# Kernel tuning notes

Measured on AMD Instinct MI355X. Metric: run time of the kernel, lower is better.

## Reference

```python
import jax, jax.numpy as jnp
import numpy as np

NEG_INF = jnp.float32(-jnp.inf)


def setup_inputs() -> dict:
    key = jax.random.key(0)
    k1, k2, k3, k4 = jax.random.split(key, 4)
    B, QL, H = 16, 32, 128          # batch, query tokens, embed dim
    N_DOCS, DL = 20000, 64          # documents, doc tokens per doc
    N_CAND = 1024                   # candidate embeddings per query
    N_EMB = N_DOCS * DL
    return {
        "q_vectors": jax.random.normal(k1, (B, QL, H), dtype=jnp.float32),
        "topk_indices": jax.random.randint(k2, (B, N_CAND), 0, N_EMB, dtype=jnp.int64),
        "vectors": jax.random.normal(k3, (N_DOCS, DL, H), dtype=jnp.float32),
        "emb2pid": jax.random.randint(k4, (N_EMB,), 0, N_DOCS, dtype=jnp.int64),
        "k": 100,
    }


def _dedup_pids(pids):
    # Emulate MaxSimPartition._get_unique_pids: unique pids per row, invalid -> -1.
    # Sort descending so any -1 entries go last, then mark duplicates as -1.
    s = -jnp.sort(-pids, axis=1)                              # [b, n] descending
    dup = jnp.concatenate(
        [jnp.zeros((s.shape[0], 1), dtype=bool), s[:, 1:] == s[:, :-1]], axis=1
    )
    return jnp.where(dup, -1, s)


def reference(q_vectors, topk_indices, vectors, emb2pid, k):
    # Map retrieved embedding rows to document pids (single partition, boundary 0).
    pids = emb2pid[topk_indices]                              # [b, n]
    n_docs = vectors.shape[0]
    pids = jnp.where((pids < 0) | (pids >= n_docs), -1, pids)
    pids = _dedup_pids(pids)                                  # [b, n]

    # Gather doc-token vectors and compute MaxSim:
    # max over doc tokens, mean over query tokens.
    d_vectors = vectors[jnp.clip(pids, 0)]                    # [b, n, d, h]
    sim = jnp.einsum("bqh,bndh->bnqd", q_vectors, d_vectors)  # [b, n, q, d]
    scores = sim.max(axis=-1).mean(axis=-1)                   # [b, n]
    scores = jnp.where(pids < 0, NEG_INF, scores)

    # Merge/top-k (single partition => one final top-k).
    k_ = min(int(k), scores.shape[-1])
    top_scores, idx = jax.lax.top_k(scores.astype(jnp.float32), k_)
    top_pids = jnp.take_along_axis(pids, idx, axis=1)
    return top_pids, top_scores
```

## Files before the change

### kernel.cpp

```cpp
#include <hip/hip_runtime.h>
#include <hip/hip_bf16.h>
#include <math.h>

#define BB   16
#define NC   1024
#define QL   32
#define HD   128
#define DLN  64
#define RK   128
#define NPW  2

typedef __attribute__((ext_vector_type(8))) short bf16x8;
typedef __attribute__((ext_vector_type(4))) float f32x4;
typedef __attribute__((ext_vector_type(4))) double f64x4;

__global__ __launch_bounds__(256) void k_qprep(
    const float* __restrict__ q, unsigned short* __restrict__ qhi)
{
    int i = blockIdx.x * 256 + threadIdx.x;
    float v = q[i];
    __hip_bfloat16 h = __float2bfloat16(v);
    qhi[i] = *reinterpret_cast<unsigned short*>(&h);
}

__global__ __launch_bounds__(1024) void k_gather_sort_dedup(
    const int* __restrict__ topk, const int* __restrict__ emb2pid,
    int n_emb, int n_docs, int* __restrict__ pids_out)
{
    const int b = blockIdx.x;
    const int t = threadIdx.x;
    __shared__ int s[NC];

    int idx = topk[b * NC + t];
    int pid = (idx >= 0 && idx < n_emb) ? emb2pid[idx] : -1;
    if (pid < 0 || pid >= n_docs) pid = -1;
    s[t] = pid;
    __syncthreads();

    for (int k2 = 2; k2 <= NC; k2 <<= 1) {
        for (int j = k2 >> 1; j > 0; j >>= 1) {
            int ixj = t ^ j;
            if (ixj > t) {
                int a = s[t], c = s[ixj];
                bool desc = ((t & k2) == 0);
                if (desc ? (a < c) : (a > c)) { s[t] = c; s[ixj] = a; }
            }
            __syncthreads();
        }
    }
    int v = s[t];
    pids_out[b * NC + t] = (t > 0 && v == s[t - 1]) ? -1 : v;
}

__device__ __forceinline__ bf16x8 cvt8(float4 a, float4 c)
{
    float v[8] = {a.x, a.y, a.z, a.w, c.x, c.y, c.z, c.w};
    bf16x8 r;
#pragma unroll
    for (int j = 0; j < 8; ++j) {
        __hip_bfloat16 h = __float2bfloat16(v[j]);
        r[j] = *reinterpret_cast<short*>(&h);
    }
    return r;
}

__global__ __launch_bounds__(256, 4) void k_screen_mfma(
    const unsigned short* __restrict__ qhi,
    const float* __restrict__ vecs,
    const int* __restrict__ pids,
    float* __restrict__ scores)
{
    const int lane = threadIdx.x & 63;
    const int wv   = threadIdx.x >> 6;
    const int bk   = blockIdx.x;
    const int BPR  = NC / (4 * NPW);
    const int b    = bk / BPR;
    const int nb   = (bk % BPR) * (4 * NPW) + wv * NPW;

    const int r16 = lane & 15;
    const int kb  = lane >> 4;

    bf16x8 qf[2][4];
#pragma unroll
    for (int m = 0; m < 2; ++m)
#pragma unroll
        for (int ks = 0; ks < 4; ++ks) {
            int off = ((b * QL + m * 16 + r16) * HD + ks * 32 + kb * 8);
            qf[m][ks] = *(const bf16x8*)(qhi + off);
        }

    for (int nn = 0; nn < NPW; ++nn) {
        const int n = nb + nn;
        const int pid = pids[b * NC + n];
        if (pid < 0) {
            if (lane == 0) scores[b * NC + n] = -__builtin_inff();
            continue;
        }
        const float* dbase = vecs + (size_t)pid * (DLN * HD);

        f32x4 acc[2][4] = {};
#pragma unroll
        for (int ks = 0; ks < 4; ++ks) {
#pragma unroll
            for (int nt = 0; nt < 4; ++nt) {
                const float* p = dbase + (nt * 16 + r16) * HD + ks * 32 + kb * 8;
                float4 x0 = *(const float4*)p;
                float4 x1 = *(const float4*)(p + 4);
                bf16x8 bh = cvt8(x0, x1);
#pragma unroll
                for (int m = 0; m < 2; ++m)
                    acc[m][nt] = __builtin_amdgcn_mfma_f32_16x16x32_bf16(
                        qf[m][ks], bh, acc[m][nt], 0, 0, 0);
            }
        }

        float s = 0.f;
#pragma unroll
        for (int m = 0; m < 2; ++m) {
#pragma unroll
            for (int r = 0; r < 4; ++r) {
                float x = fmaxf(fmaxf(acc[m][0][r], acc[m][1][r]),
                                fmaxf(acc[m][2][r], acc[m][3][r]));
                x = fmaxf(x, __shfl_xor(x, 1));
                x = fmaxf(x, __shfl_xor(x, 2));
                x = fmaxf(x, __shfl_xor(x, 4));
                x = fmaxf(x, __shfl_xor(x, 8));
                s += x;
            }
        }
        s += __shfl_xor(s, 16);
        s += __shfl_xor(s, 32);
        if (lane == 0) scores[b * NC + n] = s * (1.0f / 32.0f);
    }
}

__global__ __launch_bounds__(1024) void k_select(
    const float* __restrict__ scores, int* __restrict__ sel)
{
    const int b = blockIdx.x;
    const int t = threadIdx.x;
    __shared__ float ss[NC];
    __shared__ int   si[NC];

    ss[t] = scores[b * NC + t];
    si[t] = t;
    __syncthreads();

    for (int k2 = 2; k2 <= NC; k2 <<= 1) {
        for (int j = k2 >> 1; j > 0; j >>= 1) {
            int ixj = t ^ j;
            if (ixj > t) {
                float as = ss[t], bs = ss[ixj];
                int   ai = si[t], bi = si[ixj];
                bool a_first = (as > bs) || (as == bs && ai < bi);
                bool desc = ((t & k2) == 0);
                if (desc ? !a_first : a_first) { ss[t] = bs; si[t] = bi; ss[ixj] = as; si[ixj] = ai; }
            }
            __syncthreads();
        }
    }
    if (t < RK) sel[b * RK + t] = si[t];
}

#define DPAD (HD + 4)

__global__ __launch_bounds__(256) void k_rescore_mfma(
    const float* __restrict__ q,
    const float* __restrict__ vecs,
    const int* __restrict__ pids,
    const int* __restrict__ sel,
    double* __restrict__ resc)
{
    const int r = blockIdx.x, b = blockIdx.y;
    const int t = threadIdx.x;
    const int n = sel[b * RK + r];
    const int pid = pids[b * NC + n];
    if (pid < 0) {
        if (t == 0) resc[b * RK + r] = -__builtin_inf();
        return;
    }

    __shared__ float  sq[QL][DPAD];
    __shared__ float  sdoc[DLN][DPAD];
    __shared__ double red[4][QL];

    {
        const float4* src = (const float4*)(q + (size_t)b * QL * HD);
        for (int i = t; i < QL * HD / 4; i += 256) {
            int row = i >> 5, c4 = (i & 31) << 2;
            *(float4*)&sq[row][c4] = src[i];
        }
    }
    {
        const float4* src = (const float4*)(vecs + (size_t)pid * DLN * HD);
        for (int i = t; i < DLN * HD / 4; i += 256) {
            int row = i >> 5, c4 = (i & 31) << 2;
            *(float4*)&sdoc[row][c4] = src[i];
        }
    }
    __syncthreads();

    const int lane = t & 63;
    const int wv   = t >> 6;
    const int c16  = lane & 15;
    const int kq   = lane >> 4;

    f64x4 acc[2] = {};
#pragma unroll 4
    for (int ks = 0; ks < 32; ++ks) {
        double bv = (double)sdoc[wv * 16 + c16][ks * 4 + kq];
        double a0 = (double)sq[c16][ks * 4 + kq];
        double a1 = (double)sq[16 + c16][ks * 4 + kq];
        acc[0] = __builtin_amdgcn_mfma_f64_16x16x4f64(a0, bv, acc[0], 0, 0, 0);
        acc[1] = __builtin_amdgcn_mfma_f64_16x16x4f64(a1, bv, acc[1], 0, 0, 0);
    }

#pragma unroll
    for (int m = 0; m < 2; ++m)
#pragma unroll
        for (int rr = 0; rr < 4; ++rr) {
            double x = acc[m][rr];
            x = fmax(x, __shfl_xor(x, 1));
            x = fmax(x, __shfl_xor(x, 2));
            x = fmax(x, __shfl_xor(x, 4));
            x = fmax(x, __shfl_xor(x, 8));
            if (c16 == 0) red[wv][m * 16 + kq * 4 + rr] = x;
        }
    __syncthreads();

    if (t < 32) {
        double v = fmax(fmax(red[0][t], red[1][t]), fmax(red[2][t], red[3][t]));
        v += __shfl_xor(v, 1);
        v += __shfl_xor(v, 2);
        v += __shfl_xor(v, 4);
        v += __shfl_xor(v, 8);
        v += __shfl_xor(v, 16);
        if (t == 0) resc[b * RK + r] = v * (1.0 / 32.0);
    }
}

__global__ __launch_bounds__(RK) void k_final(
    const double* __restrict__ resc, const int* __restrict__ sel,
    const int* __restrict__ pids, float* __restrict__ out, int k)
{
    const int b = blockIdx.x;
    const int t = threadIdx.x;
    __shared__ double ss[RK];
    __shared__ int    sn[RK];

    ss[t] = resc[b * RK + t];
    sn[t] = sel[b * RK + t];
    __syncthreads();

    for (int k2 = 2; k2 <= RK; k2 <<= 1) {
        for (int j = k2 >> 1; j > 0; j >>= 1) {
            int ixj = t ^ j;
            if (ixj > t) {
                double as = ss[t], bs = ss[ixj];
                int    ai = sn[t], bi = sn[ixj];
                bool a_first = (as > bs) || (as == bs && ai < bi);
                bool desc = ((t & k2) == 0);
                if (desc ? !a_first : a_first) { ss[t] = bs; sn[t] = bi; ss[ixj] = as; sn[ixj] = ai; }
            }
            __syncthreads();
        }
    }

    if (t < k) {
        out[b * k + t]          = (float)pids[b * NC + sn[t]];
        out[BB * k + b * k + t] = (float)ss[t];
    }
}

extern "C" void kernel_launch(void* const* d_in, const int* in_sizes, int n_in,
                              void* d_out, int out_size, void* d_ws, size_t ws_size,
                              hipStream_t stream)
{
    const float* q_vectors = (const float*)d_in[0];
    const int*   topk_idx  = (const int*)d_in[1];
    const float* vectors   = (const float*)d_in[2];
    const int*   emb2pid   = (const int*)d_in[3];

    const int n_emb  = in_sizes[3];
    const int n_docs = in_sizes[2] / (DLN * HD);
    const int k      = out_size / (2 * BB);

    char* ws = (char*)d_ws;
    int*    pids_ws   = (int*)ws;      ws += BB * NC * sizeof(int);
    float*  scores_ws = (float*)ws;    ws += BB * NC * sizeof(float);
    int*    sel_ws    = (int*)ws;      ws += BB * RK * sizeof(int);
    double* resc_ws   = (double*)ws;   ws += BB * RK * sizeof(double);
    unsigned short* qhi_ws = (unsigned short*)ws;

    k_qprep<<<dim3(BB * QL * HD / 256), dim3(256), 0, stream>>>(
        q_vectors, qhi_ws);

    k_gather_sort_dedup<<<dim3(BB), dim3(NC), 0, stream>>>(
        topk_idx, emb2pid, n_emb, n_docs, pids_ws);

    k_screen_mfma<<<dim3(BB * NC / (4 * NPW)), dim3(256), 0, stream>>>(
        qhi_ws, vectors, pids_ws, scores_ws);

    k_select<<<dim3(BB), dim3(NC), 0, stream>>>(scores_ws, sel_ws);

    k_rescore_mfma<<<dim3(RK, BB), dim3(256), 0, stream>>>(
        q_vectors, vectors, pids_ws, sel_ws, resc_ws);

    k_final<<<dim3(BB), dim3(RK), 0, stream>>>(
        resc_ws, sel_ws, pids_ws, (float*)d_out, k);
}
```

Before: 167.6 us.

## Halve sort block threads, stage query in swizzled LDS, drop invalid-pid branch

The two bitonic sorts now use 512 threads, each handling one compare pair per step instead of letting half the threads sit idle. The screening kernel copies the batch's bf16 query into XOR-swizzled shared memory and loads fragments per k-step instead of holding them in registers. It also raises the occupancy hint to 5 and computes invalid pids against doc 0, masking the score afterwards. These changes aim to cut register pressure and improve latency hiding, at the cost of extra LDS traffic, a block barrier and wasted loads for invalid candidates.

Measured after the change: 172.7 us. 1.03x slower.

```diff
diff --git a/kernel.cpp b/kernel.cpp
--- a/kernel.cpp
+++ b/kernel.cpp
@@ -23,7 +23,7 @@
     qhi[i] = *reinterpret_cast<unsigned short*>(&h);
 }
 
-__global__ __launch_bounds__(1024) void k_gather_sort_dedup(
+__global__ __launch_bounds__(512) void k_gather_sort_dedup(
     const int* __restrict__ topk, const int* __restrict__ emb2pid,
     int n_emb, int n_docs, int* __restrict__ pids_out)
 {
@@ -31,25 +31,28 @@
     const int t = threadIdx.x;
     __shared__ int s[NC];
 
-    int idx = topk[b * NC + t];
-    int pid = (idx >= 0 && idx < n_emb) ? emb2pid[idx] : -1;
-    if (pid < 0 || pid >= n_docs) pid = -1;
-    s[t] = pid;
+    for (int e = t; e < NC; e += 512) {
+        int idx = topk[b * NC + e];
+        int pid = (idx >= 0 && idx < n_emb) ? emb2pid[idx] : -1;
+        if (pid < 0 || pid >= n_docs) pid = -1;
+        s[e] = pid;
+    }
     __syncthreads();
 
     for (int k2 = 2; k2 <= NC; k2 <<= 1) {
         for (int j = k2 >> 1; j > 0; j >>= 1) {
-            int ixj = t ^ j;
-            if (ixj > t) {
-                int a = s[t], c = s[ixj];
-                bool desc = ((t & k2) == 0);
-                if (desc ? (a < c) : (a > c)) { s[t] = c; s[ixj] = a; }
-            }
+            int i = ((t & ~(j - 1)) << 1) | (t & (j - 1));
+            int p = i | j;
+            int a = s[i], c = s[p];
+            bool desc = ((i & k2) == 0);
+            if (desc ? (a < c) : (a > c)) { s[i] = c; s[p] = a; }
             __syncthreads();
         }
     }
-    int v = s[t];
-    pids_out[b * NC + t] = (t > 0 && v == s[t - 1]) ? -1 : v;
+    for (int e = t; e < NC; e += 512) {
+        int v = s[e];
+        pids_out[b * NC + e] = (e > 0 && v == s[e - 1]) ? -1 : v;
+    }
 }
 
 __device__ __forceinline__ bf16x8 cvt8(float4 a, float4 c)
@@ -64,7 +67,7 @@
     return r;
 }
 
-__global__ __launch_bounds__(256, 4) void k_screen_mfma(
+__global__ __launch_bounds__(256, 5) void k_screen_mfma(
     const unsigned short* __restrict__ qhi,
     const float* __restrict__ vecs,
     const int* __restrict__ pids,
@@ -80,27 +83,34 @@
     const int r16 = lane & 15;
     const int kb  = lane >> 4;
 
-    bf16x8 qf[2][4];
-#pragma unroll
-    for (int m = 0; m < 2; ++m)
-#pragma unroll
-        for (int ks = 0; ks < 4; ++ks) {
-            int off = ((b * QL + m * 16 + r16) * HD + ks * 32 + kb * 8);
-            qf[m][ks] = *(const bf16x8*)(qhi + off);
-        }
-
+    __shared__ unsigned short sq[QL * HD];
+    {
+        const uint4* src = (const uint4*)(qhi + (size_t)b * QL * HD);
+        uint4* dst = (uint4*)sq;
+        for (int g = threadIdx.x; g < QL * HD / 8; g += 256) {
+            int row = g >> 4, col = g & 15;
+            dst[(row << 4) | (col ^ (row & 15))] = src[g];
+        }
+    }
+    __syncthreads();
+
+#pragma unroll
     for (int nn = 0; nn < NPW; ++nn) {
         const int n = nb + nn;
         const int pid = pids[b * NC + n];
-        if (pid < 0) {
-            if (lane == 0) scores[b * NC + n] = -__builtin_inff();
-            continue;
-        }
-        const float* dbase = vecs + (size_t)pid * (DLN * HD);
+        const int pidc = pid < 0 ? 0 : pid;
+        const float* dbase = vecs + (size_t)pidc * (DLN * HD);
 
         f32x4 acc[2][4] = {};
 #pragma unroll
         for (int ks = 0; ks < 4; ++ks) {
+            bf16x8 qf[2];
+#pragma unroll
+            for (int m = 0; m < 2; ++m) {
+                int row = m * 16 + r16;
+                int gr  = (ks * 4 + kb) ^ r16;
+                qf[m] = *(const bf16x8*)&sq[(row << 7) + (gr << 3)];
+            }
 #pragma unroll
             for (int nt = 0; nt < 4; ++nt) {
                 const float* p = dbase + (nt * 16 + r16) * HD + ks * 32 + kb * 8;
@@ -110,7 +120,7 @@
 #pragma unroll
                 for (int m = 0; m < 2; ++m)
                     acc[m][nt] = __builtin_amdgcn_mfma_f32_16x16x32_bf16(
-                        qf[m][ks], bh, acc[m][nt], 0, 0, 0);
+                        qf[m], bh, acc[m][nt], 0, 0, 0);
             }
         }
 
@@ -130,11 +140,13 @@
         }
         s += __shfl_xor(s, 16);
         s += __shfl_xor(s, 32);
-        if (lane == 0) scores[b * NC + n] = s * (1.0f / 32.0f);
-    }
-}
-
-__global__ __launch_bounds__(1024) void k_select(
+        if (lane == 0)
+            scores[b * NC + n] = (pid < 0) ? -__builtin_inff()
+                                           : s * (1.0f / 32.0f);
+    }
+}
+
+__global__ __launch_bounds__(512) void k_select(
     const float* __restrict__ scores, int* __restrict__ sel)
 {
     const int b = blockIdx.x;
@@ -142,19 +154,22 @@
     __shared__ float ss[NC];
     __shared__ int   si[NC];
 
-    ss[t] = scores[b * NC + t];
-    si[t] = t;
+    for (int e = t; e < NC; e += 512) {
+        ss[e] = scores[b * NC + e];
+        si[e] = e;
+    }
     __syncthreads();
 
     for (int k2 = 2; k2 <= NC; k2 <<= 1) {
         for (int j = k2 >> 1; j > 0; j >>= 1) {
-            int ixj = t ^ j;
-            if (ixj > t) {
-                float as = ss[t], bs = ss[ixj];
-                int   ai = si[t], bi = si[ixj];
-                bool a_first = (as > bs) || (as == bs && ai < bi);
-                bool desc = ((t & k2) == 0);
-                if (desc ? !a_first : a_first) { ss[t] = bs; si[t] = bi; ss[ixj] = as; si[ixj] = ai; }
+            int i = ((t & ~(j - 1)) << 1) | (t & (j - 1));
+            int p = i | j;
+            float as = ss[i], bs = ss[p];
+            int   ai = si[i], bi = si[p];
+            bool a_first = (as > bs) || (as == bs && ai < bi);
+            bool desc = ((i & k2) == 0);
+            if (desc ? !a_first : a_first) {
+                ss[i] = bs; si[i] = bi; ss[p] = as; si[p] = ai;
             }
             __syncthreads();
         }
@@ -295,13 +310,13 @@
     k_qprep<<<dim3(BB * QL * HD / 256), dim3(256), 0, stream>>>(
         q_vectors, qhi_ws);
 
-    k_gather_sort_dedup<<<dim3(BB), dim3(NC), 0, stream>>>(
+    k_gather_sort_dedup<<<dim3(BB), dim3(512), 0, stream>>>(
         topk_idx, emb2pid, n_emb, n_docs, pids_ws);
 
     k_screen_mfma<<<dim3(BB * NC / (4 * NPW)), dim3(256), 0, stream>>>(
         qhi_ws, vectors, pids_ws, scores_ws);
 
-    k_select<<<dim3(BB), dim3(NC), 0, stream>>>(scores_ws, sel_ws);
+    k_select<<<dim3(BB), dim3(512), 0, stream>>>(scores_ws, sel_ws);
 
     k_rescore_mfma<<<dim3(RK, BB), dim3(256), 0, stream>>>(
         q_vectors, vectors, pids_ws, sel_ws, resc_ws);
```
